# Kernel optimization log

Hardware: AMD Instinct MI355X
Metric: run time of the kernel (lower is better)

The kernel has to match this reference:

```python
import jax, jax.numpy as jnp
import numpy as np

N_HEAD = 16


def setup_inputs() -> dict:
    key = jax.random.key(0)
    k1, k2, k3 = jax.random.split(key, 3)
    B, T, C = 4, 2048, 1024
    x = jax.random.normal(k1, (B, T, C), dtype=jnp.float32)
    Wqkv = jax.random.normal(k2, (C, 3 * C), dtype=jnp.float32) * 0.02
    Wproj = jax.random.normal(k3, (C, C), dtype=jnp.float32) * 0.02
    return {"x": x, "Wqkv": Wqkv, "Wproj": Wproj}


def reference(x, Wqkv, Wproj):
    B, T, C = x.shape
    nh = N_HEAD
    hd = C // nh
    qkv = x @ Wqkv                                  # (B, T, 3C)
    q, k, v = jnp.split(qkv, 3, axis=-1)
    # (B, T, C) -> (B, nh, T, hd)
    q = q.reshape(B, T, nh, hd).transpose(0, 2, 1, 3)
    k = k.reshape(B, T, nh, hd).transpose(0, 2, 1, 3)
    v = v.reshape(B, T, nh, hd).transpose(0, 2, 1, 3)
    # scaled dot-product attention with causal mask (past_kv=None => T_all == T)
    att = jnp.einsum("bhtd,bhsd->bhts", q, k) / jnp.sqrt(jnp.float32(hd))
    causal = jnp.tril(jnp.ones((T, T), dtype=bool))  # (T, T)
    att = jnp.where(causal[None, None, :, :], att, jnp.float32(-jnp.inf))
    att = jax.nn.softmax(att, axis=-1)              # (B, nh, T, T)
    y = jnp.einsum("bhts,bhsd->bhtd", att, v)       # (B, nh, T, hd)
    y = y.transpose(0, 2, 1, 3).reshape(B, T, C)
    y = y @ Wproj                                   # (B, T, C)
    # present_kv (detached in original)
    return y, jax.lax.stop_gradient(k), jax.lax.stop_gradient(v)
```

## Files before the change

### kernel.cpp

```cpp
#include <hip/hip_runtime.h>
#include <hip/hip_bf16.h>


typedef __bf16 bf16;
typedef __attribute__((ext_vector_type(8))) __bf16 bf16x8;
typedef __attribute__((ext_vector_type(4))) __bf16 bf16x4;
typedef __attribute__((ext_vector_type(4))) float f32x4;

#define AS_G __attribute__((address_space(1)))
#define AS_L __attribute__((address_space(3)))

#define QSCALE 0.1803368801111204f

__device__ __forceinline__ void gld_lds16(const bf16* g, bf16* l) {
  __builtin_amdgcn_global_load_lds((const AS_G void*)g, (AS_L void*)l, 16, 0, 0);
}

__global__ __launch_bounds__(256) void k_prep(const float* __restrict__ x, bf16* __restrict__ xb,
                                              const float* __restrict__ Wqkv, bf16* __restrict__ wqkvT,
                                              const float* __restrict__ Wproj, bf16* __restrict__ wprojT) {
  __shared__ float tile[32][33];
  const int bid = blockIdx.x, tid = threadIdx.x;
  if (bid < 4096) {
    int i = (bid * 256 + tid) * 8;
    float4 a = *(const float4*)(x + i);
    float4 b = *(const float4*)(x + i + 4);
    bf16x8 o;
    o[0] = (bf16)a.x; o[1] = (bf16)a.y; o[2] = (bf16)a.z; o[3] = (bf16)a.w;
    o[4] = (bf16)b.x; o[5] = (bf16)b.y; o[6] = (bf16)b.z; o[7] = (bf16)b.w;
    *(bf16x8*)(xb + i) = o;
    return;
  }
  const float* in; bf16* out; int N, t;
  if (bid < 7168) { t = bid - 4096; N = 3072; in = Wqkv; out = wqkvT; }
  else            { t = bid - 7168; N = 1024; in = Wproj; out = wprojT; }
  const int nbx = N >> 5;
  const int bx = (t % nbx) * 32, by = (t / nbx) * 32;
  const int tx = tid & 31, ty = tid >> 5;
#pragma unroll
  for (int i = 0; i < 4; ++i)
    tile[ty + i * 8][tx] = in[(size_t)(by + ty + i * 8) * N + bx + tx];
  __syncthreads();
#pragma unroll
  for (int i = 0; i < 4; ++i)
    out[(size_t)(bx + ty + i * 8) * 1024 + by + tx] = (bf16)tile[tx][ty + i * 8];
}

__device__ __forceinline__ void gemm_main_256x128(const bf16* __restrict__ A,
                                                  const bf16* __restrict__ Bt,
                                                  int m0, int n0,
                                                  bf16* As, bf16* Bs,
                                                  f32x4 acc[4][4]) {
  const int tid = threadIdx.x;
  const int w = tid >> 6, lane = tid & 63, lo = lane & 15, hi = lane >> 4;
  const int wm = w >> 1, wn = w & 1;
  const int urow = tid >> 3;
  const int gsw = (tid & 7) ^ (urow & 7);
  const bf16* ga = A + (size_t)(m0 + urow) * 1024 + gsw * 8;
  const bf16* gb = Bt + (size_t)(n0 + urow) * 1024 + gsw * 8;
  const int p0 = hi ^ (lo & 7);
  const int aRow = wm * 64 + lo;
  const int bRow = wn * 64 + lo;

#define STAGE_A2(t, bufi, s0) do {                                                              \
    gld_lds16(ga + (size_t)(s0) * 65536 + (t) * 64,                                             \
              As + (bufi) * 16384 + (s0) * 4096 + w * 512);                                     \
    gld_lds16(ga + (size_t)((s0) + 1) * 65536 + (t) * 64,                                       \
              As + (bufi) * 16384 + ((s0) + 1) * 4096 + w * 512);                               \
  } while (0)
#define STAGE_B2(t, bufi) do {                                                                  \
    gld_lds16(gb + (t) * 64, Bs + (bufi) * 8192 + w * 512);                                     \
    gld_lds16(gb + 65536 + (t) * 64, Bs + (bufi) * 8192 + 4096 + w * 512);                      \
  } while (0)

  STAGE_A2(0, 0, 0); STAGE_A2(0, 0, 2); STAGE_B2(0, 0);
  STAGE_A2(1, 1, 0); STAGE_A2(1, 1, 2); STAGE_B2(1, 1);

  bf16x8 a[2][2], b[4][2];
  int buf = 0, sbuf = 2;
#pragma unroll 1
  for (int t = 0; t < 16; ++t) {
    if (t < 15) asm volatile("s_waitcnt vmcnt(6)" ::: "memory");
    else        asm volatile("s_waitcnt vmcnt(0)" ::: "memory");
    __builtin_amdgcn_s_barrier();
    const bf16* Ab = As + buf * 16384;
    const bf16* Bb = Bs + buf * 8192;

#pragma unroll
    for (int mi = 0; mi < 2; ++mi) {
      const bf16* r = Ab + (aRow + mi * 16) * 64;
      a[mi][0] = *(const bf16x8*)(r + p0 * 8);
      a[mi][1] = *(const bf16x8*)(r + (p0 ^ 4) * 8);
    }
#pragma unroll
    for (int ni = 0; ni < 2; ++ni) {
      const bf16* r = Bb + (bRow + ni * 16) * 64;
      b[ni][0] = *(const bf16x8*)(r + p0 * 8);
      b[ni][1] = *(const bf16x8*)(r + (p0 ^ 4) * 8);
    }
    if (t < 14) STAGE_A2(t + 2, sbuf, 0);
    __builtin_amdgcn_s_barrier();
    __builtin_amdgcn_s_setprio(1);
#pragma unroll
    for (int ks = 0; ks < 2; ++ks)
#pragma unroll
      for (int mi = 0; mi < 2; ++mi)
#pragma unroll
        for (int ni = 0; ni < 2; ++ni)
          acc[mi][ni] = __builtin_amdgcn_mfma_f32_16x16x32_bf16(a[mi][ks], b[ni][ks], acc[mi][ni], 0, 0, 0);
    __builtin_amdgcn_s_setprio(0);
    __builtin_amdgcn_s_barrier();

#pragma unroll
    for (int ni = 0; ni < 2; ++ni) {
      const bf16* r = Bb + (bRow + (ni + 2) * 16) * 64;
      b[ni + 2][0] = *(const bf16x8*)(r + p0 * 8);
      b[ni + 2][1] = *(const bf16x8*)(r + (p0 ^ 4) * 8);
    }
    if (t < 14) STAGE_A2(t + 2, sbuf, 2);
    __builtin_amdgcn_s_barrier();
    __builtin_amdgcn_s_setprio(1);
#pragma unroll
    for (int ks = 0; ks < 2; ++ks)
#pragma unroll
      for (int mi = 0; mi < 2; ++mi)
#pragma unroll
        for (int ni = 0; ni < 2; ++ni)
          acc[mi][ni + 2] = __builtin_amdgcn_mfma_f32_16x16x32_bf16(a[mi][ks], b[ni + 2][ks], acc[mi][ni + 2], 0, 0, 0);
    __builtin_amdgcn_s_setprio(0);
    __builtin_amdgcn_s_barrier();

#pragma unroll
    for (int mi = 0; mi < 2; ++mi) {
      const bf16* r = Ab + (aRow + (mi + 2) * 16) * 64;
      a[mi][0] = *(const bf16x8*)(r + p0 * 8);
      a[mi][1] = *(const bf16x8*)(r + (p0 ^ 4) * 8);
    }
    if (t < 14) STAGE_B2(t + 2, sbuf);
    __builtin_amdgcn_s_barrier();
    __builtin_amdgcn_s_setprio(1);
#pragma unroll
    for (int ks = 0; ks < 2; ++ks)
#pragma unroll
      for (int mi = 0; mi < 2; ++mi)
#pragma unroll
        for (int ni = 0; ni < 2; ++ni)
          acc[mi + 2][ni + 2] = __builtin_amdgcn_mfma_f32_16x16x32_bf16(a[mi][ks], b[ni + 2][ks], acc[mi + 2][ni + 2], 0, 0, 0);
    __builtin_amdgcn_s_setprio(0);
    __builtin_amdgcn_s_barrier();

    __builtin_amdgcn_s_setprio(1);
#pragma unroll
    for (int ks = 0; ks < 2; ++ks)
#pragma unroll
      for (int mi = 0; mi < 2; ++mi)
#pragma unroll
        for (int ni = 0; ni < 2; ++ni)
          acc[mi + 2][ni] = __builtin_amdgcn_mfma_f32_16x16x32_bf16(a[mi][ks], b[ni][ks], acc[mi + 2][ni], 0, 0, 0);
    __builtin_amdgcn_s_setprio(0);

    buf = (buf == 2) ? 0 : buf + 1;
    sbuf = (sbuf == 2) ? 0 : sbuf + 1;
  }
#undef STAGE_A2
#undef STAGE_B2
}

__global__ __launch_bounds__(512, 2) void k_gemm_qkv(const bf16* __restrict__ x,
                                                     const bf16* __restrict__ WqkvT,
                                                     bf16* __restrict__ qb, bf16* __restrict__ kb,
                                                     bf16* __restrict__ vtb,
                                                     float* __restrict__ outk, float* __restrict__ outv) {
  __shared__ bf16 As[49152], Bs[24576];
  int id = blockIdx.x;
  int swz = (id & 7) * 96 + (id >> 3);
  int by = swz / 24, bx = swz - by * 24;
  int m0 = by * 256, n0 = bx * 128;
  f32x4 acc[4][4] = {};
  gemm_main_256x128(x, WqkvT, m0, n0, As, Bs, acc);
  const int tid = threadIdx.x;
  const int w = tid >> 6, lane = tid & 63, lo = lane & 15, hi = lane >> 4;
  const int wm = w >> 1, wn = w & 1;
#pragma unroll
  for (int mi = 0; mi < 4; ++mi) {
    int growbase = m0 + wm * 64 + mi * 16 + hi * 4;
    int bb = growbase >> 11, t0 = growbase & 2047;
#pragma unroll
    for (int ni = 0; ni < 4; ++ni) {
      int gcol = n0 + wn * 64 + ni * 16 + lo;
      int part = gcol >> 10;
      int cc = gcol & 1023, h = cc >> 6, d = cc & 63;
      size_t idx0 = ((size_t)(bb * 16 + h) * 2048 + t0) * 64 + d;
      if (part == 0) {
#pragma unroll
        for (int r = 0; r < 4; ++r) qb[idx0 + (size_t)r * 64] = (bf16)(acc[mi][ni][r] * QSCALE);
      } else if (part == 1) {
#pragma unroll
        for (int r = 0; r < 4; ++r) {
          float val = acc[mi][ni][r];
          kb[idx0 + (size_t)r * 64] = (bf16)val;
          outk[idx0 + (size_t)r * 64] = val;
        }
      } else {
        bf16x4 pk;
#pragma unroll
        for (int r = 0; r < 4; ++r) {
          float val = acc[mi][ni][r];
          outv[idx0 + (size_t)r * 64] = val;
          pk[r] = (bf16)val;
        }
        *(bf16x4*)(vtb + ((size_t)(bb * 16 + h) * 64 + d) * 2048 + t0) = pk;
      }
    }
  }
}

__global__ __launch_bounds__(512, 2) void k_gemm_proj(const bf16* __restrict__ yb,
                                                      const bf16* __restrict__ WprojT,
                                                      float* __restrict__ out) {
  __shared__ bf16 As[49152], Bs[24576];
  int id = blockIdx.x;
  int swz = (id & 7) * 32 + (id >> 3);
  int by = swz >> 3, bx = swz & 7;
  int m0 = by * 256, n0 = bx * 128;
  f32x4 acc[4][4] = {};
  gemm_main_256x128(yb, WprojT, m0, n0, As, Bs, acc);
  const int tid = threadIdx.x;
  const int w = tid >> 6, lane = tid & 63, lo = lane & 15, hi = lane >> 4;
  const int wm = w >> 1, wn = w & 1;
#pragma unroll
  for (int mi = 0; mi < 4; ++mi)
#pragma unroll
    for (int ni = 0; ni < 4; ++ni)
#pragma unroll
      for (int r = 0; r < 4; ++r) {
        int grow = m0 + wm * 64 + mi * 16 + hi * 4 + r;
        int gcol = n0 + wn * 64 + ni * 16 + lo;
        out[(size_t)grow * 1024 + gcol] = acc[mi][ni][r];
      }
}

#define PSTR 76

__device__ __forceinline__ void p_store(f32x4 sacc[4], bool mask,
                                        int w, int lo, int hi, bf16* psrow) {
  if (mask) {
#pragma unroll
    for (int nt = 0; nt < 4; ++nt)
#pragma unroll
      for (int r = 0; r < 4; ++r)
        if (nt * 16 + hi * 4 + r > w * 16 + lo) sacc[nt][r] = -1e30f;
  }
#pragma unroll
  for (int nt = 0; nt < 4; ++nt) {
    bf16x4 pk;
#pragma unroll
    for (int r = 0; r < 4; ++r) pk[r] = (bf16)__builtin_amdgcn_exp2f(sacc[nt][r]);
    *(bf16x4*)(psrow + (w * 16 + lo) * PSTR + nt * 16 + hi * 4) = pk;
  }
}

__device__ __forceinline__ void write_y(bf16* __restrict__ y, int b, int h, int qrow,
                                        int hi, const f32x4 o[4], float inv) {
  size_t base = ((size_t)b * 2048 + qrow) * 1024 + h * 64;
#pragma unroll
  for (int mt = 0; mt < 4; ++mt) {
    bf16x4 yk;
#pragma unroll
    for (int r = 0; r < 4; ++r) yk[r] = (bf16)(o[mt][r] * inv);
    *(bf16x4*)(y + base + mt * 16 + hi * 4) = yk;
  }
}

__global__ __launch_bounds__(256, 4) void k_flash(const bf16* __restrict__ q,
                                                  const bf16* __restrict__ k,
                                                  const bf16* __restrict__ vt,
                                                  bf16* __restrict__ y) {
  __shared__ bf16 Ks[2 * 4096];
  __shared__ bf16 Vs[2 * 4096];
  __shared__ bf16 Ones[16 * 64];
  __shared__ bf16 Ps[128 * PSTR];
  const int bi = blockIdx.x;
  const int slot = bi >> 3;
  const int bh = (bi & 7) + 8 * (slot >> 4);
  const int j = slot & 15;
  const int jA = j, jB = 31 - j;
  const int tid = threadIdx.x, w = tid >> 6, lane = tid & 63, lo = lane & 15, hi = lane >> 4;
  const bf16* qp = q + (size_t)bh * 2048 * 64;
  const bf16* kp = k + (size_t)bh * 2048 * 64;
  const bf16* vtp = vt + (size_t)bh * 64 * 2048;

  {
    int rr = tid >> 4, c = (tid & 15) * 4;
    bf16x4 z;
    bf16 v1 = (rr == 0) ? (bf16)1.0f : (bf16)0.0f;
    z[0] = v1; z[1] = v1; z[2] = v1; z[3] = v1;
    *(bf16x4*)(Ones + rr * 64 + c) = z;
  }

#pragma unroll
  for (int p = 0; p < 2; ++p) {
    int u = tid + 256 * p;
    int row = u >> 3, g = (u & 7) ^ (row & 7);
    gld_lds16(kp + (size_t)row * 64 + g * 8, Ks + p * 2048 + w * 512);
    gld_lds16(vtp + (size_t)row * 2048 + g * 8, Vs + p * 2048 + w * 512);
  }

  bf16x8 qfA[2], qfB[2];
  {
    int qA = jA * 64 + w * 16 + lo;
    int qB = jB * 64 + w * 16 + lo;
    qfA[0] = *(const bf16x8*)(qp + (size_t)qA * 64 + hi * 8);
    qfA[1] = *(const bf16x8*)(qp + (size_t)qA * 64 + 32 + hi * 8);
    qfB[0] = *(const bf16x8*)(qp + (size_t)qB * 64 + hi * 8);
    qfB[1] = *(const bf16x8*)(qp + (size_t)qB * 64 + 32 + hi * 8);
  }
  f32x4 oA[4] = {}, oB[4] = {};
  f32x4 oLA = {}, oLB = {};

  asm volatile("s_waitcnt vmcnt(0)" ::: "memory");
  __builtin_amdgcn_s_barrier();

  for (int st = 0; st <= jB; ++st) {
    const int cb = (st & 1) * 4096;
    const int nb = cb ^ 4096;

    bf16x8 kf[4][2];
#pragma unroll
    for (int nt = 0; nt < 4; ++nt)
#pragma unroll
      for (int ks = 0; ks < 2; ++ks)
        kf[nt][ks] = *(const bf16x8*)(Ks + cb + (nt * 16 + lo) * 64 + ((ks * 4 + hi) ^ (lo & 7)) * 8);

    if (st < jB) {
      const int s1 = (st + 1) * 64;
#pragma unroll
      for (int p = 0; p < 2; ++p) {
        int u = tid + 256 * p;
        int row = u >> 3, g = (u & 7) ^ (row & 7);
        gld_lds16(kp + (size_t)(s1 + row) * 64 + g * 8, Ks + nb + p * 2048 + w * 512);
        gld_lds16(vtp + (size_t)row * 2048 + s1 + g * 8, Vs + nb + p * 2048 + w * 512);
      }
    }

    const bool actA = (st <= jA);
    f32x4 saccA[4] = {}, saccB[4] = {};
    __builtin_amdgcn_s_setprio(1);
    if (actA) {
#pragma unroll
      for (int nt = 0; nt < 4; ++nt)
#pragma unroll
        for (int ks = 0; ks < 2; ++ks)
          saccA[nt] = __builtin_amdgcn_mfma_f32_16x16x32_bf16(kf[nt][ks], qfA[ks], saccA[nt], 0, 0, 0);
    }
#pragma unroll
    for (int nt = 0; nt < 4; ++nt)
#pragma unroll
      for (int ks = 0; ks < 2; ++ks)
        saccB[nt] = __builtin_amdgcn_mfma_f32_16x16x32_bf16(kf[nt][ks], qfB[ks], saccB[nt], 0, 0, 0);
    __builtin_amdgcn_s_setprio(0);
    if (actA) p_store(saccA, st == jA, w, lo, hi, Ps);
    p_store(saccB, st == jB, w, lo, hi, Ps + 64 * PSTR);
    __asm__ volatile("s_waitcnt lgkmcnt(0)" ::: "memory");

    bf16x8 pfA[2], pfB[2];
#pragma unroll
    for (int ks = 0; ks < 2; ++ks) {
      pfB[ks] = *(const bf16x8*)(Ps + (64 + w * 16 + lo) * PSTR + ks * 32 + hi * 8);
      if (actA) pfA[ks] = *(const bf16x8*)(Ps + (w * 16 + lo) * PSTR + ks * 32 + hi * 8);
    }
    __builtin_amdgcn_s_setprio(1);
#pragma unroll
    for (int mt = 0; mt < 5; ++mt) {
#pragma unroll
      for (int ks = 0; ks < 2; ++ks) {
        int row = mt * 16 + lo;
        bf16x8 vf = (mt < 4)
            ? *(const bf16x8*)(Vs + cb + row * 64 + ((ks * 4 + hi) ^ (row & 7)) * 8)
            : *(const bf16x8*)(Ones + lo * 64 + ((ks * 4 + hi) ^ (lo & 7)) * 8);
        if (mt < 4) {
          oB[mt] = __builtin_amdgcn_mfma_f32_16x16x32_bf16(vf, pfB[ks], oB[mt], 0, 0, 0);
          if (actA) oA[mt] = __builtin_amdgcn_mfma_f32_16x16x32_bf16(vf, pfA[ks], oA[mt], 0, 0, 0);
        } else {
          oLB = __builtin_amdgcn_mfma_f32_16x16x32_bf16(vf, pfB[ks], oLB, 0, 0, 0);
          if (actA) oLA = __builtin_amdgcn_mfma_f32_16x16x32_bf16(vf, pfA[ks], oLA, 0, 0, 0);
        }
      }
    }
    __builtin_amdgcn_s_setprio(0);

    asm volatile("s_waitcnt vmcnt(0)" ::: "memory");
    __builtin_amdgcn_s_barrier();
  }

  const int b = bh >> 4, h = bh & 15;
  float lA = __shfl(oLA[0], lo, 64);
  float lB = __shfl(oLB[0], lo, 64);
  write_y(y, b, h, jA * 64 + w * 16 + lo, hi, oA, 1.0f / lA);
  write_y(y, b, h, jB * 64 + w * 16 + lo, hi, oB, 1.0f / lB);
}

extern "C" void kernel_launch(void* const* d_in, const int* in_sizes, int n_in,
                              void* d_out, int out_size, void* d_ws, size_t ws_size,
                              hipStream_t stream) {
  const float* x = (const float*)d_in[0];
  const float* Wqkv = (const float*)d_in[1];
  const float* Wproj = (const float*)d_in[2];
  float* out = (float*)d_out;

  const size_t YSZ = (size_t)8192 * 1024;
  char* ws = (char*)d_ws;
  bf16* xb = (bf16*)ws;      ws += (size_t)8192 * 1024 * 2;
  bf16* wqkvT = (bf16*)ws;   ws += (size_t)3072 * 1024 * 2;
  bf16* wprojT = (bf16*)ws;  ws += (size_t)1024 * 1024 * 2;
  bf16* qb = (bf16*)ws;      ws += (size_t)64 * 2048 * 64 * 2;
  bf16* kb = (bf16*)ws;      ws += (size_t)64 * 2048 * 64 * 2;
  bf16* vtb = (bf16*)ws;     ws += (size_t)64 * 2048 * 64 * 2;
  bf16* yb = (bf16*)ws;

  float* outy = out;
  float* outk = out + YSZ;
  float* outv = out + 2 * YSZ;

  k_prep<<<8192, 256, 0, stream>>>(x, xb, Wqkv, wqkvT, Wproj, wprojT);
  k_gemm_qkv<<<768, 512, 0, stream>>>(xb, wqkvT, qb, kb, vtb, outk, outv);
  k_flash<<<1024, 256, 0, stream>>>(qb, kb, vtb, yb);
  k_gemm_proj<<<256, 512, 0, stream>>>(yb, wprojT, outy);
}
```

Before: 301.0 us.

## Use 256x256 tiles with an 8-phase double-buffered pipeline in the QKV GEMM

Replaces the 256x128 triple-buffered QKV GEMM mainloop with a 256x256 tile whose two K-slots are double-buffered and split into eight interleaved phases of LDS reads, async global-to-LDS loads and MFMA blocks. Each wave now covers a 128x64 sub-tile, which raises arithmetic intensity per LDS byte and halves the grid to 384 blocks. The risks are higher register pressure from the 8x4 accumulators, the larger LDS footprint (128KB), and a wave-quantization change from the smaller grid. The waitcnt and barrier macros elsewhere are only cosmetic.

```diff
diff --git a/kernel.cpp b/kernel.cpp
--- a/kernel.cpp
+++ b/kernel.cpp
@@ -15,6 +15,10 @@
 __device__ __forceinline__ void gld_lds16(const bf16* g, bf16* l) {
   __builtin_amdgcn_global_load_lds((const AS_G void*)g, (AS_L void*)l, 16, 0, 0);
 }
+
+#define BAR() __builtin_amdgcn_s_barrier()
+#define LGKM0() asm volatile("s_waitcnt lgkmcnt(0)" ::: "memory")
+#define VMC(n) asm volatile("s_waitcnt vmcnt(" #n ")" ::: "memory")
 
 __global__ __launch_bounds__(256) void k_prep(const float* __restrict__ x, bf16* __restrict__ xb,
                                               const float* __restrict__ Wqkv, bf16* __restrict__ wqkvT,
@@ -44,6 +48,153 @@
 #pragma unroll
   for (int i = 0; i < 4; ++i)
     out[(size_t)(bx + ty + i * 8) * 1024 + by + tx] = (bf16)tile[tx][ty + i * 8];
+}
+
+__device__ __forceinline__ void gemm_core_8ph(const bf16* __restrict__ A,
+                                              const bf16* __restrict__ Bt,
+                                              int m0, int n0,
+                                              bf16* As, bf16* Bs,
+                                              f32x4 acc[8][4]) {
+  const int tid = threadIdx.x;
+  const int w = tid >> 6, lane = tid & 63, lo = lane & 15, hi = lane >> 4;
+  const int wm = w >> 2, wn = w & 3;
+  const int row64 = tid >> 3;
+  const int g = (tid & 7) ^ (row64 & 7);
+  const bf16* ga = A + (size_t)(m0 + row64) * 1024 + g * 8;
+  const bf16* gb = Bt + (size_t)(n0 + row64) * 1024 + g * 8;
+  bf16* Ad = As + tid * 8;
+  bf16* Bd = Bs + tid * 8;
+  const int aoff = (wm * 128 + lo) * 64;
+  const int boff = (wn * 64 + lo) * 64;
+  const int sw0 = (hi ^ (lo & 7)) * 8;
+  const int sw1 = ((4 + hi) ^ (lo & 7)) * 8;
+
+#define SGA(kt, s, slot) gld_lds16(ga + (size_t)(s) * 65536 + (size_t)(kt) * 64, Ad + (slot) * 16384 + (s) * 4096)
+#define SGB(kt, s, slot) gld_lds16(gb + (size_t)(s) * 65536 + (size_t)(kt) * 64, Bd + (slot) * 16384 + (s) * 4096)
+#define RDA(dst, slot, mi, ks) dst = *(const bf16x8*)(As + (slot) * 16384 + aoff + (mi) * 1024 + ((ks) ? sw1 : sw0))
+#define RDB(dst, slot, ni, ks) dst = *(const bf16x8*)(Bs + (slot) * 16384 + boff + (ni) * 1024 + ((ks) ? sw1 : sw0))
+#define MM16(mb, nb, AF, BF)                                                            \
+  _Pragma("unroll") for (int ks = 0; ks < 2; ++ks)                                      \
+  _Pragma("unroll") for (int mi = 0; mi < 4; ++mi)                                      \
+  _Pragma("unroll") for (int ni = 0; ni < 2; ++ni)                                      \
+    acc[(mb) + mi][(nb) + ni] = __builtin_amdgcn_mfma_f32_16x16x32_bf16(                \
+        AF[mi][ks], BF[ni][ks], acc[(mb) + mi][(nb) + ni], 0, 0, 0);
+
+  SGA(0, 0, 0); SGA(0, 1, 0); SGA(0, 2, 0); SGA(0, 3, 0);
+  SGB(0, 0, 0); SGB(0, 1, 0); SGB(0, 2, 0); SGB(0, 3, 0);
+  SGA(1, 0, 1); SGA(1, 1, 1); SGA(1, 2, 1); SGA(1, 3, 1);
+  VMC(4); BAR();
+
+  bf16x8 aL[4][2], aH[4][2], bb[2][2];
+#pragma unroll 1
+  for (int it = 0; it < 8; ++it) {
+    const int o1 = 2 * it + 1, e2 = 2 * it + 2, o2 = 2 * it + 3;
+    const bool st = (it < 7);
+#pragma unroll
+    for (int mi = 0; mi < 4; ++mi) { RDA(aL[mi][0], 0, mi, 0); RDA(aL[mi][1], 0, mi, 1); }
+#pragma unroll
+    for (int ni = 0; ni < 2; ++ni) { RDB(bb[ni][0], 0, ni, 0); RDB(bb[ni][1], 0, ni, 1); }
+    SGB(o1, 0, 1); SGB(o1, 1, 1);
+    BAR(); LGKM0();
+    __builtin_amdgcn_s_setprio(1); MM16(0, 0, aL, bb); __builtin_amdgcn_s_setprio(0);
+    BAR();
+#pragma unroll
+    for (int mi = 0; mi < 4; ++mi) { RDA(aH[mi][0], 0, 4 + mi, 0); RDA(aH[mi][1], 0, 4 + mi, 1); }
+    SGB(o1, 2, 1); SGB(o1, 3, 1);
+    BAR(); LGKM0();
+    __builtin_amdgcn_s_setprio(1); MM16(4, 0, aH, bb); __builtin_amdgcn_s_setprio(0);
+    BAR();
+#pragma unroll
+    for (int ni = 0; ni < 2; ++ni) { RDB(bb[ni][0], 0, 2 + ni, 0); RDB(bb[ni][1], 0, 2 + ni, 1); }
+    if (st) { SGA(e2, 0, 0); SGA(e2, 1, 0); }
+    BAR(); LGKM0();
+    __builtin_amdgcn_s_setprio(1); MM16(4, 2, aH, bb); __builtin_amdgcn_s_setprio(0);
+    BAR();
+    if (st) { SGA(e2, 2, 0); SGA(e2, 3, 0); }
+    BAR(); LGKM0();
+    __builtin_amdgcn_s_setprio(1); MM16(0, 2, aL, bb); __builtin_amdgcn_s_setprio(0);
+    if (st) { VMC(4); } else { VMC(0); }
+    BAR();
+#pragma unroll
+    for (int mi = 0; mi < 4; ++mi) { RDA(aL[mi][0], 1, mi, 0); RDA(aL[mi][1], 1, mi, 1); }
+#pragma unroll
+    for (int ni = 0; ni < 2; ++ni) { RDB(bb[ni][0], 1, ni, 0); RDB(bb[ni][1], 1, ni, 1); }
+    if (st) { SGB(e2, 0, 0); SGB(e2, 1, 0); }
+    BAR(); LGKM0();
+    __builtin_amdgcn_s_setprio(1); MM16(0, 0, aL, bb); __builtin_amdgcn_s_setprio(0);
+    BAR();
+#pragma unroll
+    for (int mi = 0; mi < 4; ++mi) { RDA(aH[mi][0], 1, 4 + mi, 0); RDA(aH[mi][1], 1, 4 + mi, 1); }
+    if (st) { SGB(e2, 2, 0); SGB(e2, 3, 0); }
+    BAR(); LGKM0();
+    __builtin_amdgcn_s_setprio(1); MM16(4, 0, aH, bb); __builtin_amdgcn_s_setprio(0);
+    BAR();
+#pragma unroll
+    for (int ni = 0; ni < 2; ++ni) { RDB(bb[ni][0], 1, 2 + ni, 0); RDB(bb[ni][1], 1, 2 + ni, 1); }
+    if (st) { SGA(o2, 0, 1); SGA(o2, 1, 1); }
+    BAR(); LGKM0();
+    __builtin_amdgcn_s_setprio(1); MM16(4, 2, aH, bb); __builtin_amdgcn_s_setprio(0);
+    BAR();
+    if (st) { SGA(o2, 2, 1); SGA(o2, 3, 1); }
+    BAR(); LGKM0();
+    __builtin_amdgcn_s_setprio(1); MM16(0, 2, aL, bb); __builtin_amdgcn_s_setprio(0);
+    if (st) { VMC(4); } else { VMC(0); }
+    BAR();
+  }
+#undef SGA
+#undef SGB
+#undef RDA
+#undef RDB
+#undef MM16
+}
+
+__global__ __launch_bounds__(512, 2) void k_gemm_qkv(const bf16* __restrict__ x,
+                                                     const bf16* __restrict__ WqkvT,
+                                                     bf16* __restrict__ qb, bf16* __restrict__ kb,
+                                                     bf16* __restrict__ vtb,
+                                                     float* __restrict__ outk, float* __restrict__ outv) {
+  __shared__ bf16 As[32768], Bs[32768];
+  int id = blockIdx.x;
+  int swz = (id & 7) * 48 + (id >> 3);
+  int by = swz / 12, bx = swz - by * 12;
+  int m0 = by * 256, n0 = bx * 256;
+  f32x4 acc[8][4] = {};
+  gemm_core_8ph(x, WqkvT, m0, n0, As, Bs, acc);
+  const int tid = threadIdx.x;
+  const int w = tid >> 6, lane = tid & 63, lo = lane & 15, hi = lane >> 4;
+  const int wm = w >> 2, wn = w & 3;
+#pragma unroll
+  for (int mi = 0; mi < 8; ++mi) {
+    int growbase = m0 + wm * 128 + mi * 16 + hi * 4;
+    int bb = growbase >> 11, t0 = growbase & 2047;
+#pragma unroll
+    for (int ni = 0; ni < 4; ++ni) {
+      int gcol = n0 + wn * 64 + ni * 16 + lo;
+      int part = gcol >> 10;
+      int cc = gcol & 1023, h = cc >> 6, d = cc & 63;
+      size_t idx0 = ((size_t)(bb * 16 + h) * 2048 + t0) * 64 + d;
+      if (part == 0) {
+#pragma unroll
+        for (int r = 0; r < 4; ++r) qb[idx0 + (size_t)r * 64] = (bf16)(acc[mi][ni][r] * QSCALE);
+      } else if (part == 1) {
+#pragma unroll
+        for (int r = 0; r < 4; ++r) {
+          float val = acc[mi][ni][r];
+          kb[idx0 + (size_t)r * 64] = (bf16)val;
+          outk[idx0 + (size_t)r * 64] = val;
+        }
+      } else {
+        bf16x4 pk;
+#pragma unroll
+        for (int r = 0; r < 4; ++r) {
+          float val = acc[mi][ni][r];
+          outv[idx0 + (size_t)r * 64] = val;
+          pk[r] = (bf16)val;
+        }
+        *(bf16x4*)(vtb + ((size_t)(bb * 16 + h) * 64 + d) * 2048 + t0) = pk;
+      }
+    }
+  }
 }
 
 __device__ __forceinline__ void gemm_main_256x128(const bf16* __restrict__ A,
@@ -80,9 +231,8 @@
   int buf = 0, sbuf = 2;
 #pragma unroll 1
   for (int t = 0; t < 16; ++t) {
-    if (t < 15) asm volatile("s_waitcnt vmcnt(6)" ::: "memory");
-    else        asm volatile("s_waitcnt vmcnt(0)" ::: "memory");
-    __builtin_amdgcn_s_barrier();
+    if (t < 15) { VMC(6); } else { VMC(0); }
+    BAR();
     const bf16* Ab = As + buf * 16384;
     const bf16* Bb = Bs + buf * 8192;
 
@@ -99,7 +249,7 @@
       b[ni][1] = *(const bf16x8*)(r + (p0 ^ 4) * 8);
     }
     if (t < 14) STAGE_A2(t + 2, sbuf, 0);
-    __builtin_amdgcn_s_barrier();
+    BAR();
     __builtin_amdgcn_s_setprio(1);
 #pragma unroll
     for (int ks = 0; ks < 2; ++ks)
@@ -109,7 +259,7 @@
         for (int ni = 0; ni < 2; ++ni)
           acc[mi][ni] = __builtin_amdgcn_mfma_f32_16x16x32_bf16(a[mi][ks], b[ni][ks], acc[mi][ni], 0, 0, 0);
     __builtin_amdgcn_s_setprio(0);
-    __builtin_amdgcn_s_barrier();
+    BAR();
 
 #pragma unroll
     for (int ni = 0; ni < 2; ++ni) {
@@ -118,7 +268,7 @@
       b[ni + 2][1] = *(const bf16x8*)(r + (p0 ^ 4) * 8);
     }
     if (t < 14) STAGE_A2(t + 2, sbuf, 2);
-    __builtin_amdgcn_s_barrier();
+    BAR();
     __builtin_amdgcn_s_setprio(1);
 #pragma unroll
     for (int ks = 0; ks < 2; ++ks)
@@ -128,7 +278,7 @@
         for (int ni = 0; ni < 2; ++ni)
           acc[mi][ni + 2] = __builtin_amdgcn_mfma_f32_16x16x32_bf16(a[mi][ks], b[ni + 2][ks], acc[mi][ni + 2], 0, 0, 0);
     __builtin_amdgcn_s_setprio(0);
-    __builtin_amdgcn_s_barrier();
+    BAR();
 
 #pragma unroll
     for (int mi = 0; mi < 2; ++mi) {
@@ -137,7 +287,7 @@
       a[mi][1] = *(const bf16x8*)(r + (p0 ^ 4) * 8);
     }
     if (t < 14) STAGE_B2(t + 2, sbuf);
-    __builtin_amdgcn_s_barrier();
+    BAR();
     __builtin_amdgcn_s_setprio(1);
 #pragma unroll
     for (int ks = 0; ks < 2; ++ks)
@@ -147,7 +297,7 @@
         for (int ni = 0; ni < 2; ++ni)
           acc[mi + 2][ni + 2] = __builtin_amdgcn_mfma_f32_16x16x32_bf16(a[mi][ks], b[ni + 2][ks], acc[mi + 2][ni + 2], 0, 0, 0);
     __builtin_amdgcn_s_setprio(0);
-    __builtin_amdgcn_s_barrier();
+    BAR();
 
     __builtin_amdgcn_s_setprio(1);
 #pragma unroll
@@ -164,55 +314,6 @@
   }
 #undef STAGE_A2
 #undef STAGE_B2
-}
-
-__global__ __launch_bounds__(512, 2) void k_gemm_qkv(const bf16* __restrict__ x,
-                                                     const bf16* __restrict__ WqkvT,
-                                                     bf16* __restrict__ qb, bf16* __restrict__ kb,
-                                                     bf16* __restrict__ vtb,
-                                                     float* __restrict__ outk, float* __restrict__ outv) {
-  __shared__ bf16 As[49152], Bs[24576];
-  int id = blockIdx.x;
-  int swz = (id & 7) * 96 + (id >> 3);
-  int by = swz / 24, bx = swz - by * 24;
-  int m0 = by * 256, n0 = bx * 128;
-  f32x4 acc[4][4] = {};
-  gemm_main_256x128(x, WqkvT, m0, n0, As, Bs, acc);
-  const int tid = threadIdx.x;
-  const int w = tid >> 6, lane = tid & 63, lo = lane & 15, hi = lane >> 4;
-  const int wm = w >> 1, wn = w & 1;
-#pragma unroll
-  for (int mi = 0; mi < 4; ++mi) {
-    int growbase = m0 + wm * 64 + mi * 16 + hi * 4;
-    int bb = growbase >> 11, t0 = growbase & 2047;
-#pragma unroll
-    for (int ni = 0; ni < 4; ++ni) {
-      int gcol = n0 + wn * 64 + ni * 16 + lo;
-      int part = gcol >> 10;
-      int cc = gcol & 1023, h = cc >> 6, d = cc & 63;
-      size_t idx0 = ((size_t)(bb * 16 + h) * 2048 + t0) * 64 + d;
-      if (part == 0) {
-#pragma unroll
-        for (int r = 0; r < 4; ++r) qb[idx0 + (size_t)r * 64] = (bf16)(acc[mi][ni][r] * QSCALE);
-      } else if (part == 1) {
-#pragma unroll
-        for (int r = 0; r < 4; ++r) {
-          float val = acc[mi][ni][r];
-          kb[idx0 + (size_t)r * 64] = (bf16)val;
-          outk[idx0 + (size_t)r * 64] = val;
-        }
-      } else {
-        bf16x4 pk;
-#pragma unroll
-        for (int r = 0; r < 4; ++r) {
-          float val = acc[mi][ni][r];
-          outv[idx0 + (size_t)r * 64] = val;
-          pk[r] = (bf16)val;
-        }
-        *(bf16x4*)(vtb + ((size_t)(bb * 16 + h) * 64 + d) * 2048 + t0) = pk;
-      }
-    }
-  }
 }
 
 __global__ __launch_bounds__(512, 2) void k_gemm_proj(const bf16* __restrict__ yb,
@@ -318,8 +419,8 @@
   f32x4 oA[4] = {}, oB[4] = {};
   f32x4 oLA = {}, oLB = {};
 
-  asm volatile("s_waitcnt vmcnt(0)" ::: "memory");
-  __builtin_amdgcn_s_barrier();
+  VMC(0);
+  BAR();
 
   for (int st = 0; st <= jB; ++st) {
     const int cb = (st & 1) * 4096;
@@ -361,7 +462,7 @@
     __builtin_amdgcn_s_setprio(0);
     if (actA) p_store(saccA, st == jA, w, lo, hi, Ps);
     p_store(saccB, st == jB, w, lo, hi, Ps + 64 * PSTR);
-    __asm__ volatile("s_waitcnt lgkmcnt(0)" ::: "memory");
+    LGKM0();
 
     bf16x8 pfA[2], pfB[2];
 #pragma unroll
@@ -389,8 +490,8 @@
     }
     __builtin_amdgcn_s_setprio(0);
 
-    asm volatile("s_waitcnt vmcnt(0)" ::: "memory");
-    __builtin_amdgcn_s_barrier();
+    VMC(0);
+    BAR();
   }
 
   const int b = bh >> 4, h = bh & 15;
@@ -423,7 +524,7 @@
   float* outv = out + 2 * YSZ;
 
   k_prep<<<8192, 256, 0, stream>>>(x, xb, Wqkv, wqkvT, Wproj, wprojT);
-  k_gemm_qkv<<<768, 512, 0, stream>>>(xb, wqkvT, qb, kb, vtb, outk, outv);
+  k_gemm_qkv<<<384, 512, 0, stream>>>(xb, wqkvT, qb, kb, vtb, outk, outv);
   k_flash<<<1024, 256, 0, stream>>>(qb, kb, vtb, yb);
   k_gemm_proj<<<256, 512, 0, stream>>>(yb, wprojT, outy);
 }
```

Result: no change. 304.1 us (+1.0%).
